# Performance work log

Measured on AMD Instinct MI355X. Metric: run time of the kernel, lower is better.

Reference implementation:

```python
import jax, jax.numpy as jnp
import numpy as np

LK = 8  # db4 has 8 taps
LEVEL = 5
# pywt.Wavelet('db4').filter_bank[0] == dec_lo
DB4_LO = np.array([-0.010597401784997278, 0.032883011666982945, 0.030841381835986965,
                   -0.18703481171888114, -0.02798376941698385, 0.6308807679295904,
                   0.7148465705525415, 0.23037781330885523], dtype=np.float32)
DN = ('NCH', 'OIH', 'NCH')


def _wpt_kernels(level):
    # Filter_Free WPT: distinct kernel per child node; parent j even -> (lp, hp), odd -> (hp, lp)
    cmf = (-1.0) ** np.arange(LK)
    k_lp = DB4_LO
    k_hp = (DB4_LO[::-1] * cmf).astype(np.float32)
    ks = []
    for i in range(level):
        rows = []
        for j in range(2 ** i):
            rows += [k_lp, k_hp] if j % 2 == 0 else [k_hp, k_lp]
        ks.append(jnp.asarray(np.stack(rows)))  # [2^(i+1), LK]
    return ks


def setup_inputs() -> dict:
    key = jax.random.key(0)
    kx, kb = jax.random.split(key)
    B, N = 128, 32768
    inp = {'x': jax.random.normal(kx, (B, 1, N), dtype=jnp.float32)}
    for i, K in enumerate(_wpt_kernels(LEVEL)):
        inp[f'k{i + 1}'] = K
    for i in range(LEVEL):
        kb, sub = jax.random.split(kb)
        # small positive thresholds (Act_Init=0 would make the threshold an exact identity)
        inp[f'b{i + 1}'] = 0.1 * jax.random.uniform(sub, (2 ** (i + 1),), dtype=jnp.float32)
    return inp


def _analysis(c, K, b):
    # c: [B, G, M] parents -> [B, 2G, M//2] children; one grouped 8-tap conv for the whole level
    G = c.shape[1]
    cp = jnp.pad(c, ((0, 0), (0, 0), (LK // 2 - 1, LK // 2)))
    y = jax.lax.conv_general_dilated(cp, K[:, None, :], (2,), 'VALID',
                                     feature_group_count=G, dimension_numbers=DN)
    bb = b[None, :, None]
    # symmetric sigmoid soft-threshold (Thresh_SigSym), fused elementwise
    return y * (jax.nn.sigmoid(10.0 * (y - bb)) + jax.nn.sigmoid(-10.0 * (y + bb)))


def _synthesis(y, K):
    # adjoint of the strided analysis conv (conv_transpose): [B, 2G, M] -> [B, G, 2M]
    G = y.shape[1] // 2
    M = y.shape[2]
    W = jnp.flip(K, -1).reshape(G, 2, LK)  # sum the two children of each parent
    out = jax.lax.conv_general_dilated(y, W, (1,), [(LK - 1, LK - 1)], lhs_dilation=(2,),
                                       feature_group_count=G, dimension_numbers=DN)
    pl = LK // 2 - 1  # undo analysis left pad
    return out[:, :, pl:pl + 2 * M]


def reference(x, k1, k2, k3, k4, k5, b1, b2, b3, b4, b5):
    Ks = [k1, k2, k3, k4, k5]
    bs = [b1, b2, b3, b4, b5]
    c = x  # [B, 1, N]
    for K, b in zip(Ks, bs):
        c = _analysis(c, K, b)
    for K in Ks[::-1]:
        c = _synthesis(c, K)
    return c  # [B, 1, N] reconstruction
```

## Files before the change

### kernel.cpp

```cpp
#include <hip/hip_runtime.h>

#define TPB 256

constexpr int NSEQ = 32768;
constexpr int C0   = 2048;
constexpr float SCG = 14.4269504089f;


__device__ __forceinline__ float4 ldf4(const float* p) { return *reinterpret_cast<const float4*>(p); }
__device__ __forceinline__ void   stf4(float* p, const float4 v) { *reinterpret_cast<float4*>(p) = v; }

__device__ __forceinline__ float rfl(float x) {
    return __builtin_bit_cast(float, __builtin_amdgcn_readfirstlane(__builtin_bit_cast(int, x)));
}

__device__ __forceinline__ float gated(float y, float tb) {
    float e1 = __builtin_amdgcn_exp2f(fmaf(y, -SCG, tb));
    float e2 = __builtin_amdgcn_exp2f(fmaf(y,  SCG, tb));
    return y * (__builtin_amdgcn_rcpf(1.f + e1) + __builtin_amdgcn_rcpf(1.f + e2));
}

template<int LEin, int LEout, int P, int PAIRS, int Nlev, int BOFF, bool EDGE, bool LAST>
__device__ __forceinline__ void analysis8(
    const float* __restrict__ in, float* __restrict__ out,
    const float* __restrict__ lp, const float* __restrict__ hp,
    const float* __restrict__ bias, int outBase)
{
    constexpr int TPC = P / 8;
    constexpr int TOT = PAIRS * TPC;
    for (int task = threadIdx.x; task < TOT; task += TPB) {
        const int c  = task / TPC;
        const int i0 = (task - c * TPC) * 8;

        const float* pe = in + c * (2 * LEin);
        const float* pa = BOFF ? (pe + LEin) : pe;
        const float* pb = BOFF ? pe : (pe + LEin);

        float a[12], b[12];
        reinterpret_cast<float4*>(a)[0] = ldf4(pa + i0);
        reinterpret_cast<float4*>(a)[1] = ldf4(pa + i0 + 4);
        reinterpret_cast<float4*>(a)[2] = ldf4(pa + i0 + 8);
        reinterpret_cast<float4*>(b)[0] = ldf4(pb + i0);
        reinterpret_cast<float4*>(b)[1] = ldf4(pb + i0 + 4);
        reinterpret_cast<float4*>(b)[2] = ldf4(pb + i0 + 8);

        const int sw     = c & 1;
        const int ch_lp  = 2 * c + sw;
        const int ch_hp  = 2 * c + 1 - sw;
        const float tb_l = bias[ch_lp];
        const float tb_h = bias[ch_hp];

        float vl[8], vh[8];
#pragma unroll
        for (int r = 0; r < 8; ++r) {
            float yl = 0.f, yh = 0.f;
#pragma unroll
            for (int u = 0; u < 4; ++u) {
                yl = fmaf(a[r + u], lp[2 * u], yl);
                yl = fmaf(b[r + BOFF + u], lp[2 * u + 1], yl);
                yh = fmaf(a[r + u], hp[2 * u], yh);
                yh = fmaf(b[r + BOFF + u], hp[2 * u + 1], yh);
            }
            float wl = gated(yl, tb_l);
            float wh = gated(yh, tb_h);
            if (EDGE) {
                const bool ok = ((unsigned)(outBase + i0 + r) < (unsigned)Nlev);
                wl = ok ? wl : 0.f;
                wh = ok ? wh : 0.f;
            }
            vl[r] = wl; vh[r] = wh;
        }

        if (LAST) {
            float* ol = out + ch_lp * LEout + i0;
            float* oh = out + ch_hp * LEout + i0;
            stf4(ol,     make_float4(vl[0], vl[1], vl[2], vl[3]));
            stf4(ol + 4, make_float4(vl[4], vl[5], vl[6], vl[7]));
            stf4(oh,     make_float4(vh[0], vh[1], vh[2], vh[3]));
            stf4(oh + 4, make_float4(vh[4], vh[5], vh[6], vh[7]));
        } else {
            const int j0 = i0 >> 1;
            float* ol = out + ch_lp * (2 * LEout);
            float* oh = out + ch_hp * (2 * LEout);
            stf4(ol + j0,         make_float4(vl[0], vl[2], vl[4], vl[6]));
            stf4(ol + LEout + j0, make_float4(vl[1], vl[3], vl[5], vl[7]));
            stf4(oh + j0,         make_float4(vh[0], vh[2], vh[4], vh[6]));
            stf4(oh + LEout + j0, make_float4(vh[1], vh[3], vh[5], vh[7]));
        }
    }
}

template<int Sin, int Sout, int P, int G, int Nlev, bool EDGE>
__device__ __forceinline__ void synth8(
    const float* __restrict__ in, float* __restrict__ out,
    const float* __restrict__ lp, const float* __restrict__ hp, int outBase)
{
    constexpr int TPG = P / 8;
    constexpr int TOT = G * TPG;
    for (int task = threadIdx.x; task < TOT; task += TPB) {
        const int g   = task / TPG;
        const int nl0 = (task - g * TPG) * 8;
        const int sw  = g & 1;

        float ya[8], yb[8];
        {
            const float* p0 = in + (2 * g + sw)     * Sin + nl0 / 2;
            const float* p1 = in + (2 * g + 1 - sw) * Sin + nl0 / 2;
            reinterpret_cast<float4*>(ya)[0] = ldf4(p0);
            reinterpret_cast<float4*>(ya)[1] = ldf4(p0 + 4);
            reinterpret_cast<float4*>(yb)[0] = ldf4(p1);
            reinterpret_cast<float4*>(yb)[1] = ldf4(p1 + 4);
        }

        float o[8];
#pragma unroll
        for (int r = 0; r < 8; ++r) {
            const int jr = (r + 1) >> 1;
            const int kb = 7 - (r & 1);
            float acc = 0.f;
#pragma unroll
            for (int q = 0; q < 4; ++q) {
                acc = fmaf(ya[jr + q], lp[kb - 2 * q], acc);
                acc = fmaf(yb[jr + q], hp[kb - 2 * q], acc);
            }
            if (EDGE) {
                const bool ok = ((unsigned)(outBase + nl0 + r) < (unsigned)Nlev);
                acc = ok ? acc : 0.f;
            }
            o[r] = acc;
        }
        float* op = out + g * Sout + nl0;
        stf4(op,     make_float4(o[0], o[1], o[2], o[3]));
        stf4(op + 4, make_float4(o[4], o[5], o[6], o[7]));
    }
}

template<bool EDGE>
__device__ __forceinline__ void run_chunk(
    const float* __restrict__ xb, float* __restrict__ ob, int s,
    float* __restrict__ bufA, float* __restrict__ bufB,
    const float* __restrict__ lp, const float* __restrict__ hp,
    const float* __restrict__ bss)
{
    const int tid = threadIdx.x;

    {
        const int b0 = s - 222;
        if (EDGE) {
            for (int t = tid; t < 626; t += TPB) {
                const int g = b0 + 4 * t;
                const float e0 = ((unsigned)g       < (unsigned)NSEQ) ? xb[g]     : 0.f;
                const float o0 = ((unsigned)(g + 1) < (unsigned)NSEQ) ? xb[g + 1] : 0.f;
                const float e1 = ((unsigned)(g + 2) < (unsigned)NSEQ) ? xb[g + 2] : 0.f;
                const float o1 = ((unsigned)(g + 3) < (unsigned)NSEQ) ? xb[g + 3] : 0.f;
                *reinterpret_cast<float2*>(bufA + 2 * t)        = make_float2(e0, e1);
                *reinterpret_cast<float2*>(bufA + 1252 + 2 * t) = make_float2(o0, o1);
            }
        } else {
            for (int t = tid; t < 626; t += TPB) {
                const float* p = xb + b0 + 4 * t;
                const float2 fa = *reinterpret_cast<const float2*>(p);
                const float2 fb = *reinterpret_cast<const float2*>(p + 2);
                *reinterpret_cast<float2*>(bufA + 2 * t)        = make_float2(fa.x, fb.x);
                *reinterpret_cast<float2*>(bufA + 1252 + 2 * t) = make_float2(fa.y, fb.y);
            }
        }
    }
    __syncthreads();

    analysis8<1252, 628, 1248,  1, 16384, 1, EDGE, false>(bufA, bufB, lp, hp, bss + 0,  (s >> 1) - 109);
    __syncthreads();
    analysis8< 628, 316,  624,  2,  8192, 0, EDGE, false>(bufB, bufA, lp, hp, bss + 2,  (s >> 2) - 53);
    __syncthreads();
    analysis8< 316, 156,  312,  4,  4096, 0, EDGE, false>(bufA, bufB, lp, hp, bss + 6,  (s >> 3) - 25);
    __syncthreads();
    analysis8< 156,  76,  152,  8,  2048, 0, EDGE, false>(bufB, bufA, lp, hp, bss + 14, (s >> 4) - 11);
    __syncthreads();
    analysis8<  76,  72,   72, 16,  1024, 0, EDGE, true >(bufA, bufB, lp, hp, bss + 30, (s >> 5) - 4);
    __syncthreads();

    synth8<  72,  136,  136, 16,  2048, EDGE>(bufB, bufA, lp, hp, (s >> 4) - 4);
    __syncthreads();
    synth8< 136,  264,  264,  8,  4096, EDGE>(bufA, bufB, lp, hp, (s >> 3) - 4);
    __syncthreads();
    synth8< 264,  520,  520,  4,  8192, EDGE>(bufB, bufA, lp, hp, (s >> 2) - 4);
    __syncthreads();
    synth8< 520, 1032, 1032,  2, 16384, EDGE>(bufA, bufB, lp, hp, (s >> 1) - 4);
    __syncthreads();

    {
        const int i0 = tid * 8;
        float ya[12], yb[12];
        {
            const float* p0 = bufB + i0 / 2;
            const float* p1 = p0 + 1032;
            reinterpret_cast<float4*>(ya)[0] = ldf4(p0);
            reinterpret_cast<float4*>(ya)[1] = ldf4(p0 + 4);
            reinterpret_cast<float4*>(ya)[2] = ldf4(p0 + 8);
            reinterpret_cast<float4*>(yb)[0] = ldf4(p1);
            reinterpret_cast<float4*>(yb)[1] = ldf4(p1 + 4);
            reinterpret_cast<float4*>(yb)[2] = ldf4(p1 + 8);
        }
        float o[8];
#pragma unroll
        for (int r = 0; r < 8; ++r) {
            const int jr = ((r + 1) >> 1) + 2;
            const int kb = 7 - (r & 1);
            float acc = 0.f;
#pragma unroll
            for (int q = 0; q < 4; ++q) {
                acc = fmaf(ya[jr + q], lp[kb - 2 * q], acc);
                acc = fmaf(yb[jr + q], hp[kb - 2 * q], acc);
            }
            o[r] = acc;
        }
        stf4(ob + i0,     make_float4(o[0], o[1], o[2], o[3]));
        stf4(ob + i0 + 4, make_float4(o[4], o[5], o[6], o[7]));
    }
}

__global__ __launch_bounds__(TPB, 8) void wpt_fused(
    const float* __restrict__ x,
    const float* __restrict__ K1, const float* __restrict__ K2,
    const float* __restrict__ K3, const float* __restrict__ K4,
    const float* __restrict__ K5,
    const float* __restrict__ B1, const float* __restrict__ B2,
    const float* __restrict__ B3, const float* __restrict__ B4,
    const float* __restrict__ B5,
    float* __restrict__ out)
{
    __shared__ __align__(16) float bufA[2528];
    __shared__ __align__(16) float bufB[2512];
    __shared__ float bss[62];

    const int tid   = threadIdx.x;
    const int batch = blockIdx.x >> 4;
    const int cid   = blockIdx.x & 15;
    const int s     = cid * C0;

    float lp[8], hp[8];
#pragma unroll
    for (int t = 0; t < 8; ++t) {
        lp[t] = rfl(K1[t]);
        hp[t] = rfl(K1[8 + t]);
    }

    {
        const float* bin[5] = {B1, B2, B3, B4, B5};
        const int boff[5] = {0, 2, 6, 14, 30};
#pragma unroll
        for (int l = 0; l < 5; ++l)
            for (int i = tid; i < (2 << l); i += TPB) bss[boff[l] + i] = SCG * bin[l][i];
    }

    const float* xb = x + batch * NSEQ;
    float* ob = out + batch * NSEQ + s;

    if (cid == 0 || cid == 15)
        run_chunk<true >(xb, ob, s, bufA, bufB, lp, hp, bss);
    else
        run_chunk<false>(xb, ob, s, bufA, bufB, lp, hp, bss);
}

extern "C" void kernel_launch(void* const* d_in, const int* in_sizes, int n_in,
                              void* d_out, int out_size, void* d_ws, size_t ws_size,
                              hipStream_t stream) {
    const int nbatch = in_sizes[0] / NSEQ;
    wpt_fused<<<dim3(nbatch * (NSEQ / C0)), dim3(TPB), 0, stream>>>(
        (const float*)d_in[0],
        (const float*)d_in[1], (const float*)d_in[2],
        (const float*)d_in[3], (const float*)d_in[4],
        (const float*)d_in[5],
        (const float*)d_in[6], (const float*)d_in[7],
        (const float*)d_in[8], (const float*)d_in[9],
        (const float*)d_in[10],
        (float*)d_out);
}
```

Measured before the change: 120.6 us.

## Halve chunk size and block size with 4-output analysis tasks

Reduces each block's chunk from 2048 to 1024 samples and threads per block from 256 to 128, resizing the shared buffers and level geometry to match. Analysis now computes 4 outputs per task from plain even/odd split buffers, and the input is loaded with scalar loads. The aim is more blocks and lower LDS use per block for better occupancy and balance. The cost is a larger relative halo, meaning more redundant loads and compute per output sample.

Measured after the change: 121.1 us. About the same (+0.4%).

```diff
diff --git a/kernel.cpp b/kernel.cpp
--- a/kernel.cpp
+++ b/kernel.cpp
@@ -1,9 +1,9 @@
 #include <hip/hip_runtime.h>
 
-#define TPB 256
+#define TPB 128
 
 constexpr int NSEQ = 32768;
-constexpr int C0   = 2048;
+constexpr int C0   = 1024;
 constexpr float SCG = 14.4269504089f;
 
 
@@ -20,29 +20,25 @@
     return y * (__builtin_amdgcn_rcpf(1.f + e1) + __builtin_amdgcn_rcpf(1.f + e2));
 }
 
-template<int LEin, int LEout, int P, int PAIRS, int Nlev, int BOFF, bool EDGE, bool LAST>
-__device__ __forceinline__ void analysis8(
+template<int LEin, int LEout, int P, int PAIRS, int Nlev, bool EDGE, bool LAST>
+__device__ __forceinline__ void analysis4(
     const float* __restrict__ in, float* __restrict__ out,
     const float* __restrict__ lp, const float* __restrict__ hp,
     const float* __restrict__ bias, int outBase)
 {
-    constexpr int TPC = P / 8;
+    constexpr int TPC = P / 4;
     constexpr int TOT = PAIRS * TPC;
     for (int task = threadIdx.x; task < TOT; task += TPB) {
         const int c  = task / TPC;
-        const int i0 = (task - c * TPC) * 8;
-
-        const float* pe = in + c * (2 * LEin);
-        const float* pa = BOFF ? (pe + LEin) : pe;
-        const float* pb = BOFF ? pe : (pe + LEin);
-
-        float a[12], b[12];
-        reinterpret_cast<float4*>(a)[0] = ldf4(pa + i0);
-        reinterpret_cast<float4*>(a)[1] = ldf4(pa + i0 + 4);
-        reinterpret_cast<float4*>(a)[2] = ldf4(pa + i0 + 8);
-        reinterpret_cast<float4*>(b)[0] = ldf4(pb + i0);
-        reinterpret_cast<float4*>(b)[1] = ldf4(pb + i0 + 4);
-        reinterpret_cast<float4*>(b)[2] = ldf4(pb + i0 + 8);
+        const int i0 = (task - c * TPC) * 4;
+
+        const float* pe = in + c * (2 * LEin) + i0;
+        const float* po = pe + LEin;
+        float a[8], b[8];
+        reinterpret_cast<float4*>(a)[0] = ldf4(pe);
+        reinterpret_cast<float4*>(a)[1] = ldf4(pe + 4);
+        reinterpret_cast<float4*>(b)[0] = ldf4(po);
+        reinterpret_cast<float4*>(b)[1] = ldf4(po + 4);
 
         const int sw     = c & 1;
         const int ch_lp  = 2 * c + sw;
@@ -50,16 +46,16 @@
         const float tb_l = bias[ch_lp];
         const float tb_h = bias[ch_hp];
 
-        float vl[8], vh[8];
-#pragma unroll
-        for (int r = 0; r < 8; ++r) {
+        float vl[4], vh[4];
+#pragma unroll
+        for (int r = 0; r < 4; ++r) {
             float yl = 0.f, yh = 0.f;
 #pragma unroll
             for (int u = 0; u < 4; ++u) {
                 yl = fmaf(a[r + u], lp[2 * u], yl);
-                yl = fmaf(b[r + BOFF + u], lp[2 * u + 1], yl);
+                yl = fmaf(b[r + u], lp[2 * u + 1], yl);
                 yh = fmaf(a[r + u], hp[2 * u], yh);
-                yh = fmaf(b[r + BOFF + u], hp[2 * u + 1], yh);
+                yh = fmaf(b[r + u], hp[2 * u + 1], yh);
             }
             float wl = gated(yl, tb_l);
             float wh = gated(yh, tb_h);
@@ -72,30 +68,26 @@
         }
 
         if (LAST) {
-            float* ol = out + ch_lp * LEout + i0;
-            float* oh = out + ch_hp * LEout + i0;
-            stf4(ol,     make_float4(vl[0], vl[1], vl[2], vl[3]));
-            stf4(ol + 4, make_float4(vl[4], vl[5], vl[6], vl[7]));
-            stf4(oh,     make_float4(vh[0], vh[1], vh[2], vh[3]));
-            stf4(oh + 4, make_float4(vh[4], vh[5], vh[6], vh[7]));
+            stf4(out + ch_lp * LEout + i0, make_float4(vl[0], vl[1], vl[2], vl[3]));
+            stf4(out + ch_hp * LEout + i0, make_float4(vh[0], vh[1], vh[2], vh[3]));
         } else {
             const int j0 = i0 >> 1;
             float* ol = out + ch_lp * (2 * LEout);
             float* oh = out + ch_hp * (2 * LEout);
-            stf4(ol + j0,         make_float4(vl[0], vl[2], vl[4], vl[6]));
-            stf4(ol + LEout + j0, make_float4(vl[1], vl[3], vl[5], vl[7]));
-            stf4(oh + j0,         make_float4(vh[0], vh[2], vh[4], vh[6]));
-            stf4(oh + LEout + j0, make_float4(vh[1], vh[3], vh[5], vh[7]));
-        }
-    }
-}
-
-template<int Sin, int Sout, int P, int G, int Nlev, bool EDGE>
+            *reinterpret_cast<float2*>(ol + j0)         = make_float2(vl[0], vl[2]);
+            *reinterpret_cast<float2*>(ol + LEout + j0) = make_float2(vl[1], vl[3]);
+            *reinterpret_cast<float2*>(oh + j0)         = make_float2(vh[0], vh[2]);
+            *reinterpret_cast<float2*>(oh + LEout + j0) = make_float2(vh[1], vh[3]);
+        }
+    }
+}
+
+template<int Sin, int Sout, int G, int Nlev, bool EDGE>
 __device__ __forceinline__ void synth8(
     const float* __restrict__ in, float* __restrict__ out,
     const float* __restrict__ lp, const float* __restrict__ hp, int outBase)
 {
-    constexpr int TPG = P / 8;
+    constexpr int TPG = Sout / 8;
     constexpr int TOT = G * TPG;
     for (int task = threadIdx.x; task < TOT; task += TPB) {
         const int g   = task / TPG;
@@ -145,47 +137,38 @@
     const int tid = threadIdx.x;
 
     {
-        const int b0 = s - 222;
-        if (EDGE) {
-            for (int t = tid; t < 626; t += TPB) {
-                const int g = b0 + 4 * t;
-                const float e0 = ((unsigned)g       < (unsigned)NSEQ) ? xb[g]     : 0.f;
-                const float o0 = ((unsigned)(g + 1) < (unsigned)NSEQ) ? xb[g + 1] : 0.f;
-                const float e1 = ((unsigned)(g + 2) < (unsigned)NSEQ) ? xb[g + 2] : 0.f;
-                const float o1 = ((unsigned)(g + 3) < (unsigned)NSEQ) ? xb[g + 3] : 0.f;
-                *reinterpret_cast<float2*>(bufA + 2 * t)        = make_float2(e0, e1);
-                *reinterpret_cast<float2*>(bufA + 1252 + 2 * t) = make_float2(o0, o1);
-            }
-        } else {
-            for (int t = tid; t < 626; t += TPB) {
-                const float* p = xb + b0 + 4 * t;
-                const float2 fa = *reinterpret_cast<const float2*>(p);
-                const float2 fb = *reinterpret_cast<const float2*>(p + 2);
-                *reinterpret_cast<float2*>(bufA + 2 * t)        = make_float2(fa.x, fb.x);
-                *reinterpret_cast<float2*>(bufA + 1252 + 2 * t) = make_float2(fa.y, fb.y);
-            }
-        }
-    }
-    __syncthreads();
-
-    analysis8<1252, 628, 1248,  1, 16384, 1, EDGE, false>(bufA, bufB, lp, hp, bss + 0,  (s >> 1) - 109);
-    __syncthreads();
-    analysis8< 628, 316,  624,  2,  8192, 0, EDGE, false>(bufB, bufA, lp, hp, bss + 2,  (s >> 2) - 53);
-    __syncthreads();
-    analysis8< 316, 156,  312,  4,  4096, 0, EDGE, false>(bufA, bufB, lp, hp, bss + 6,  (s >> 3) - 25);
-    __syncthreads();
-    analysis8< 156,  76,  152,  8,  2048, 0, EDGE, false>(bufB, bufA, lp, hp, bss + 14, (s >> 4) - 11);
-    __syncthreads();
-    analysis8<  76,  72,   72, 16,  1024, 0, EDGE, true >(bufA, bufB, lp, hp, bss + 30, (s >> 5) - 4);
-    __syncthreads();
-
-    synth8<  72,  136,  136, 16,  2048, EDGE>(bufB, bufA, lp, hp, (s >> 4) - 4);
-    __syncthreads();
-    synth8< 136,  264,  264,  8,  4096, EDGE>(bufA, bufB, lp, hp, (s >> 3) - 4);
-    __syncthreads();
-    synth8< 264,  520,  520,  4,  8192, EDGE>(bufB, bufA, lp, hp, (s >> 2) - 4);
-    __syncthreads();
-    synth8< 520, 1032, 1032,  2, 16384, EDGE>(bufA, bufB, lp, hp, (s >> 1) - 4);
+        const int base = s - 221;
+        for (int j = tid; j < 764; j += TPB) {
+            const int g0 = base + 2 * j;
+            if (EDGE) {
+                bufA[j]       = ((unsigned)g0       < (unsigned)NSEQ) ? xb[g0]     : 0.f;
+                bufA[764 + j] = ((unsigned)(g0 + 1) < (unsigned)NSEQ) ? xb[g0 + 1] : 0.f;
+            } else {
+                bufA[j]       = xb[g0];
+                bufA[764 + j] = xb[g0 + 1];
+            }
+        }
+    }
+    __syncthreads();
+
+    analysis4<764, 380, 760,  1, 16384, EDGE, false>(bufA, bufB, lp, hp, bss + 0,  (s >> 1) - 109);
+    __syncthreads();
+    analysis4<380, 188, 376,  2,  8192, EDGE, false>(bufB, bufA, lp, hp, bss + 2,  (s >> 2) - 53);
+    __syncthreads();
+    analysis4<188,  92, 184,  4,  4096, EDGE, false>(bufA, bufB, lp, hp, bss + 6,  (s >> 3) - 25);
+    __syncthreads();
+    analysis4< 92,  44,  88,  8,  2048, EDGE, false>(bufB, bufA, lp, hp, bss + 14, (s >> 4) - 11);
+    __syncthreads();
+    analysis4< 44,  40,  40, 16,  1024, EDGE, true >(bufA, bufB, lp, hp, bss + 30, (s >> 5) - 4);
+    __syncthreads();
+
+    synth8< 40,  72, 16,  2048, EDGE>(bufB, bufA, lp, hp, (s >> 4) - 4);
+    __syncthreads();
+    synth8< 72, 136,  8,  4096, EDGE>(bufA, bufB, lp, hp, (s >> 3) - 4);
+    __syncthreads();
+    synth8<136, 264,  4,  8192, EDGE>(bufB, bufA, lp, hp, (s >> 2) - 4);
+    __syncthreads();
+    synth8<264, 520,  2, 16384, EDGE>(bufA, bufB, lp, hp, (s >> 1) - 4);
     __syncthreads();
 
     {
@@ -193,7 +176,7 @@
         float ya[12], yb[12];
         {
             const float* p0 = bufB + i0 / 2;
-            const float* p1 = p0 + 1032;
+            const float* p1 = p0 + 520;
             reinterpret_cast<float4*>(ya)[0] = ldf4(p0);
             reinterpret_cast<float4*>(ya)[1] = ldf4(p0 + 4);
             reinterpret_cast<float4*>(ya)[2] = ldf4(p0 + 8);
@@ -229,13 +212,13 @@
     const float* __restrict__ B5,
     float* __restrict__ out)
 {
-    __shared__ __align__(16) float bufA[2528];
-    __shared__ __align__(16) float bufB[2512];
+    __shared__ __align__(16) float bufA[1528];
+    __shared__ __align__(16) float bufB[1520];
     __shared__ float bss[62];
 
     const int tid   = threadIdx.x;
-    const int batch = blockIdx.x >> 4;
-    const int cid   = blockIdx.x & 15;
+    const int batch = blockIdx.x >> 5;
+    const int cid   = blockIdx.x & 31;
     const int s     = cid * C0;
 
     float lp[8], hp[8];
@@ -256,7 +239,7 @@
     const float* xb = x + batch * NSEQ;
     float* ob = out + batch * NSEQ + s;
 
-    if (cid == 0 || cid == 15)
+    if (cid == 0 || cid == 31)
         run_chunk<true >(xb, ob, s, bufA, bufB, lp, hp, bss);
     else
         run_chunk<false>(xb, ob, s, bufA, bufB, lp, hp, bss);
```
